# Kernel optimization log

Hardware: AMD Instinct MI355X
Metric: run time of the kernel (lower is better)

The kernel has to match this reference:

```python
import jax, jax.numpy as jnp
import numpy as np

N = 50000
E = 800000
EPS = 1e-5
# per-layer (in_dim, heads, out_dim, concat) matching GraphEncoder defaults
LAYERS = [(16, 4, 32, True), (128, 4, 32, True), (128, 4, 32, True), (128, 1, 128, False)]


def setup_inputs() -> dict:
    key = jax.random.key(0)
    ks = jax.random.split(key, 32)
    rn = lambda k, shape: jax.random.normal(k, shape, jnp.float32) * 0.1
    inp = {}
    inp["node_types"] = jax.random.randint(ks[0], (N,), 0, 3)
    inp["edge_index"] = jax.random.randint(ks[1], (2, E), 0, N)
    inp["emb"] = rn(ks[2], (3, 16))
    i = 3
    for li, (ind, h, od, _) in enumerate(LAYERS):
        inp[f"Wl{li}"] = rn(ks[i], (ind, h * od)); i += 1
        inp[f"Wr{li}"] = rn(ks[i], (ind, h * od)); i += 1
        inp[f"att{li}"] = rn(ks[i], (h, od)); i += 1
        inp[f"b{li}"] = rn(ks[i], (h * od if li < 3 else od,)); i += 1
    inp["ln_g"] = jnp.ones((4, 128), jnp.float32)
    inp["ln_b"] = jnp.zeros((4, 128), jnp.float32)
    return inp


def gatv2_layer(x, src, dst, Wl, Wr, att, b, heads, out_dim, concat):
    # PyG GATv2Conv (share_weights=False, negative_slope=0.2, self-loops added by caller)
    n = x.shape[0]
    xl = (x @ Wl).reshape(n, heads, out_dim)  # source transform (messages)
    xr = (x @ Wr).reshape(n, heads, out_dim)  # target transform
    e = jax.nn.leaky_relu(xl[src] + xr[dst], 0.2)          # [E', H, D]
    logit = jnp.einsum('ehd,hd->eh', e, att)               # [E', H]
    lmax = jax.ops.segment_max(logit, dst, num_segments=n)  # segment softmax over dst
    p = jnp.exp(logit - lmax[dst])
    z = jax.ops.segment_sum(p, dst, num_segments=n)
    alpha = p / z[dst]                                      # every node has a self-loop -> z > 0
    out = jax.ops.segment_sum(xl[src] * alpha[..., None], dst, num_segments=n)  # [n, H, D]
    out = out.reshape(n, heads * out_dim) if concat else out.mean(axis=1)
    return out + b


def layer_norm(x, g, b):
    mu = x.mean(-1, keepdims=True)
    var = ((x - mu) ** 2).mean(-1, keepdims=True)
    return (x - mu) / jnp.sqrt(var + EPS) * g + b


def reference(node_types, edge_index, emb, Wl0, Wr0, att0, b0, Wl1, Wr1, att1, b1,
              Wl2, Wr2, att2, b2, Wl3, Wr3, att3, b3, ln_g, ln_b):
    n = node_types.shape[0]
    loops = jnp.arange(n)
    src = jnp.concatenate([edge_index[0], loops])
    dst = jnp.concatenate([edge_index[1], loops])
    x = emb[node_types]
    params = [(Wl0, Wr0, att0, b0), (Wl1, Wr1, att1, b1), (Wl2, Wr2, att2, b2), (Wl3, Wr3, att3, b3)]
    for li, ((Wl, Wr, att, b), (_, h, od, concat)) in enumerate(zip(params, LAYERS)):
        res = x
        x = gatv2_layer(x, src, dst, Wl, Wr, att, b, h, od, concat)
        if x.shape[-1] == res.shape[-1]:
            x = x + res
        x = jax.nn.relu(layer_norm(x, ln_g[li], ln_b[li]))
    return x
```

## Files before the change

### kernel.cpp

```cpp
#include <hip/hip_runtime.h>

__global__ void GraphEncoder_20555713479231_kernel() {}

using hfrag8 = __attribute__((ext_vector_type(8))) _Float16;
using facc4  = __attribute__((ext_vector_type(4))) float;
using h2     = __attribute__((ext_vector_type(2))) _Float16;

__device__ __forceinline__ unsigned short f2h_bits(float f) {
  union { _Float16 h; unsigned short u; } c;
  c.h = (_Float16)f;
  return c.u;
}
__device__ __forceinline__ unsigned packh(float a, float b) {
  return (unsigned)f2h_bits(a) | ((unsigned)f2h_bits(b) << 16);
}
__device__ __forceinline__ h2 u2h(unsigned u) {
  union { unsigned u; h2 h; } c;
  c.u = u;
  return c.h;
}
__device__ __forceinline__ unsigned h22u(h2 h) {
  union { h2 h; unsigned u; } c;
  c.h = h;
  return c.u;
}
__device__ __forceinline__ float h2f_lo(unsigned u) { return (float)u2h(u).x; }
__device__ __forceinline__ float h2f_hi(unsigned u) { return (float)u2h(u).y; }

__global__ __launch_bounds__(256) void k_hist(const int* __restrict__ dst,
                                              int* __restrict__ deg, int e) {
  int i = blockIdx.x * blockDim.x + threadIdx.x;
  if (i < e) atomicAdd(&deg[dst[i]], 1);
}

__global__ __launch_bounds__(256) void k_scan1(const int* __restrict__ deg,
                                               int* __restrict__ off,
                                               int* __restrict__ bsum, int n) {
  __shared__ int wsum[4];
  int tid = threadIdx.x;
  int gid = blockIdx.x * 256 + tid;
  int lane = tid & 63, wid = tid >> 6;
  int v = (gid < n) ? (deg[gid] + 1) : 0;
  int x = v;
  #pragma unroll
  for (int d = 1; d < 64; d <<= 1) {
    int t = __shfl_up(x, d);
    if (lane >= d) x += t;
  }
  if (lane == 63) wsum[wid] = x;
  __syncthreads();
  int wpre = 0;
  for (int k = 0; k < wid; ++k) wpre += wsum[k];
  if (gid < n) off[gid] = wpre + x - v;
  if (tid == 0) {
    int t = 0;
    #pragma unroll
    for (int k = 0; k < 4; ++k) t += wsum[k];
    bsum[blockIdx.x] = t;
  }
}

__global__ __launch_bounds__(256) void k_scan2(int* __restrict__ bsum,
                                               int* __restrict__ off, int nb, int n) {
  __shared__ int wsum[4];
  int tid = threadIdx.x;
  int lane = tid & 63, wid = tid >> 6;
  int v = (tid < nb) ? bsum[tid] : 0;
  int x = v;
  #pragma unroll
  for (int d = 1; d < 64; d <<= 1) {
    int t = __shfl_up(x, d);
    if (lane >= d) x += t;
  }
  if (lane == 63) wsum[wid] = x;
  __syncthreads();
  int wpre = 0;
  for (int k = 0; k < wid; ++k) wpre += wsum[k];
  if (tid < nb) bsum[tid] = wpre + x - v;
  if (tid == 0) {
    int t = 0;
    #pragma unroll
    for (int k = 0; k < 4; ++k) t += wsum[k];
    off[n] = t;
  }
}

__global__ __launch_bounds__(256) void k_scan3(int* __restrict__ off,
                                               const int* __restrict__ bsum,
                                               int* __restrict__ pos,
                                               int* __restrict__ csr, int n) {
  int gid = blockIdx.x * 256 + threadIdx.x;
  if (gid < n) {
    int o = off[gid] + bsum[blockIdx.x];
    off[gid] = o;
    csr[o] = gid;
    pos[gid] = o + 1;
  }
}

__global__ __launch_bounds__(256) void k_fill(const int* __restrict__ src,
                                              const int* __restrict__ dst,
                                              int* __restrict__ pos,
                                              int* __restrict__ csr, int e) {
  int i = blockIdx.x * blockDim.x + threadIdx.x;
  if (i < e) {
    int d = dst[i];
    int p = atomicAdd(&pos[d], 1);
    csr[p] = src[i];
  }
}

__global__ __launch_bounds__(256)
void k_pack3(const float* __restrict__ wl1, const float* __restrict__ wr1,
             const float* __restrict__ wl2, const float* __restrict__ wr2,
             const float* __restrict__ wl3, const float* __restrict__ wr3,
             const float* __restrict__ emb,
             const float* __restrict__ wl0, const float* __restrict__ wr0,
             const int* __restrict__ types, int n,
             unsigned short* __restrict__ bp,
             unsigned* __restrict__ tlb, float* __restrict__ trf,
             unsigned* __restrict__ ptypes) {
  int b = blockIdx.x;
  if (b < 384) {
    int idx = b * 256 + threadIdx.x;
    int layer = idx >> 15;
    int r = idx & 32767;
    int j = r & 7, lane = (r >> 3) & 63, ct = (r >> 9) & 15, t = r >> 13;
    int k = t * 32 + (lane >> 4) * 8 + j;
    int c = ct * 16 + (lane & 15);
    const float* wl = (layer == 0) ? wl1 : ((layer == 1) ? wl2 : wl3);
    const float* wr = (layer == 0) ? wr1 : ((layer == 1) ? wr2 : wr3);
    float v = (c < 128) ? wl[k * 128 + c] : wr[k * 128 + (c - 128)];
    bp[idx] = f2h_bits(v);
  } else if (b == 384) {
    int tid = threadIdx.x;
    if (tid >= 192) return;
    int row = tid >> 6, cp = tid & 63, c0 = cp * 2;
    float al0 = 0.f, al1 = 0.f, ar0 = 0.f, ar1 = 0.f;
    #pragma unroll
    for (int k = 0; k < 16; ++k) {
      float ev = emb[row * 16 + k];
      al0 += ev * wl0[k * 128 + c0];
      al1 += ev * wl0[k * 128 + c0 + 1];
      ar0 += ev * wr0[k * 128 + c0];
      ar1 += ev * wr0[k * 128 + c0 + 1];
    }
    tlb[row * 64 + cp] = packh(al0, al1);
    *(float2*)(trf + row * 128 + c0) = make_float2(ar0, ar1);
  } else {
    int i = (b - 385) * 256 + threadIdx.x;
    int npk = (n + 15) >> 4;
    if (i < npk) {
      unsigned pw = 0;
      #pragma unroll
      for (int j = 0; j < 16; ++j) {
        int u = i * 16 + j;
        int ty = (u < n) ? (types[u] & 3) : 3;
        pw |= ((unsigned)ty) << (2 * j);
      }
      ptypes[i] = pw;
    }
  }
}

__global__ __launch_bounds__(256)
void k_agg0(const int* __restrict__ off, const int* __restrict__ csr,
            const unsigned* __restrict__ ptypes,
            const unsigned* __restrict__ tlb, const float* __restrict__ trf,
            const float* __restrict__ att, const float* __restrict__ bias,
            const float* __restrict__ lng, const float* __restrict__ lnb,
            unsigned* __restrict__ yout, int n) {
  int v = (blockIdx.x * blockDim.x + threadIdx.x) >> 6;
  int lane = threadIdx.x & 63;
  if (v >= n) return;
  v = __builtin_amdgcn_readfirstlane(v);
  int beg = off[v], end = off[v + 1];
  int c0 = 0, c1 = 0, c2 = 0;
  for (int base = beg; base < end; base += 64) {
    int e = base + lane;
    bool act = e < end;
    int u = act ? csr[e] : 0;
    unsigned pw = ptypes[u >> 4];
    int ty = act ? (int)((pw >> ((u & 15) * 2)) & 3) : 3;
    c0 += __popcll(__ballot(ty == 0));
    c1 += __popcll(__ballot(ty == 1));
    c2 += __popcll(__ballot(ty == 2));
  }
  float cnt[3] = {(float)c0, (float)c1, (float)c2};
  int f0 = lane * 2;
  unsigned pwv = ptypes[v >> 4];
  int tyv = (int)((pwv >> ((v & 15) * 2)) & 3);
  float2 xrv = *(const float2*)(trf + tyv * 128 + f0);
  float a0 = att[f0], a1 = att[f0 + 1];
  float s = 0.f, O0 = 0.f, O1 = 0.f;
  #pragma unroll
  for (int ty = 0; ty < 3; ++ty) {
    unsigned p = tlb[ty * 64 + lane];
    float x0 = h2f_lo(p), x1 = h2f_hi(p);
    float t0 = x0 + xrv.x; t0 = t0 > 0.f ? t0 : 0.2f * t0;
    float t1 = x1 + xrv.y; t1 = t1 > 0.f ? t1 : 0.2f * t1;
    float c = t0 * a0 + t1 * a1;
    c += __shfl_xor(c, 1);
    c += __shfl_xor(c, 2);
    c += __shfl_xor(c, 4);
    c += __shfl_xor(c, 8);
    float w = cnt[ty] * __expf(c);
    s += w;
    O0 = fmaf(w, x0, O0);
    O1 = fmaf(w, x1, O1);
  }
  float inv = 1.f / s;
  float o0 = O0 * inv + bias[f0];
  float o1 = O1 * inv + bias[f0 + 1];
  float sum = o0 + o1, sq = o0 * o0 + o1 * o1;
  #pragma unroll
  for (int d2 = 1; d2 < 64; d2 <<= 1) {
    sum += __shfl_xor(sum, d2);
    sq += __shfl_xor(sq, d2);
  }
  float mu = sum * (1.f / 128.f);
  float var = sq * (1.f / 128.f) - mu * mu;
  float rstd = rsqrtf(var + 1e-5f);
  float y0 = fmaxf((o0 - mu) * rstd * lng[f0] + lnb[f0], 0.f);
  float y1 = fmaxf((o1 - mu) * rstd * lng[f0 + 1] + lnb[f0 + 1], 0.f);
  yout[(size_t)v * 64 + lane] = packh(y0, y1);
}

__global__ __launch_bounds__(256)
void k_gemm(const unsigned* __restrict__ x, const unsigned short* __restrict__ bp,
            unsigned* __restrict__ xlo, unsigned* __restrict__ xro, int nstrips, int n) {
  int wave = (blockIdx.x * 256 + threadIdx.x) >> 6;
  int lane = threadIdx.x & 63;
  if (wave >= nstrips) return;
  int r0 = wave * 16;
  int row = r0 + (lane & 15);
  if (row >= n) row = n - 1;
  int quad = lane >> 4;
  const unsigned* ap = x + (size_t)row * 64;
  hfrag8 a[4];
  #pragma unroll
  for (int t = 0; t < 4; ++t) a[t] = *(const hfrag8*)(ap + t * 16 + quad * 4);
  unsigned short* xloS = (unsigned short*)xlo;
  unsigned short* xroS = (unsigned short*)xro;
  int rbase = r0 + quad * 4;
  #pragma unroll
  for (int ct = 0; ct < 16; ++ct) {
    facc4 acc = {0.f, 0.f, 0.f, 0.f};
    #pragma unroll
    for (int t = 0; t < 4; ++t) {
      hfrag8 b = *(const hfrag8*)(bp + (size_t)(((t * 16 + ct) * 64 + lane) * 8));
      acc = __builtin_amdgcn_mfma_f32_16x16x32_f16(a[t], b, acc, 0, 0, 0);
    }
    int col = (ct & 7) * 16 + (lane & 15);
    unsigned short* dstp = (ct < 8) ? xloS : xroS;
    #pragma unroll
    for (int i = 0; i < 4; ++i) {
      int r = rbase + i;
      if (r < n) dstp[(size_t)r * 128 + col] = f2h_bits(acc[i]);
    }
  }
}

__global__ __launch_bounds__(256)
void k_agg(const int* __restrict__ off, const int* __restrict__ csr,
           const unsigned* __restrict__ xl, const unsigned* __restrict__ xr,
           const float* __restrict__ att, const float* __restrict__ bias,
           const unsigned* __restrict__ xres,
           const float* __restrict__ lng, const float* __restrict__ lnb,
           unsigned* __restrict__ ybf, float* __restrict__ yf32, int n, int wide) {
  int v = (blockIdx.x * blockDim.x + threadIdx.x) >> 6;
  int lane = threadIdx.x & 63;
  if (v >= n) return;
  v = __builtin_amdgcn_readfirstlane(v);
  int f0 = lane * 2;
  h2 a2;
  a2.x = (_Float16)att[f0];
  a2.y = (_Float16)att[f0 + 1];
  h2 r2 = u2h(xr[(size_t)v * 64 + lane]);
  h2 k02 = {(_Float16)0.2f, (_Float16)0.2f};
  int beg = off[v], end = off[v + 1];
  int last = end - 1;
  const unsigned* xlp = xl + lane;
  int iA = csr[beg];
  int iB = csr[min(beg + 1, last)];
  int iC = csr[min(beg + 2, last)];
  int iD = csr[min(beg + 3, last)];
  unsigned pA = xlp[(size_t)iA * 64];
  unsigned pB = xlp[(size_t)iB * 64];
  unsigned pC = xlp[(size_t)iC * 64];
  unsigned pD = xlp[(size_t)iD * 64];
  float sa = 0.f, sb = 0.f;
  h2 Oa = {(_Float16)0.f, (_Float16)0.f};
  h2 Ob = {(_Float16)0.f, (_Float16)0.f};
  for (int e = beg; e < end; e += 2) {
    int i4 = csr[min(e + 4, last)];
    int i5 = csr[min(e + 5, last)];
    unsigned p4 = xlp[(size_t)i4 * 64];
    unsigned p5 = xlp[(size_t)i5 * 64];
    h2 xa = u2h(pA), xb = u2h(pB);
    h2 ta = xa + r2;
    h2 tb = xb + r2;
    h2 la = __builtin_elementwise_max(ta, ta * k02);
    h2 lb = __builtin_elementwise_max(tb, tb * k02);
    h2 da = la * a2;
    h2 db = lb * a2;
    h2 cp;
    cp.x = da.x + da.y;
    cp.y = db.x + db.y;
    unsigned cu = h22u(cp);
    cu = h22u(u2h(cu) + u2h((unsigned)__shfl_xor((int)cu, 1)));
    cu = h22u(u2h(cu) + u2h((unsigned)__shfl_xor((int)cu, 2)));
    cu = h22u(u2h(cu) + u2h((unsigned)__shfl_xor((int)cu, 4)));
    cu = h22u(u2h(cu) + u2h((unsigned)__shfl_xor((int)cu, 8)));
    if (wide) {
      cu = h22u(u2h(cu) + u2h((unsigned)__shfl_xor((int)cu, 16)));
      cu = h22u(u2h(cu) + u2h((unsigned)__shfl_xor((int)cu, 32)));
    }
    h2 cf = u2h(cu);
    float wa = __expf((float)cf.x);
    float wb = (e + 1 < end) ? __expf((float)cf.y) : 0.f;
    sa += wa;
    sb += wb;
    _Float16 wah = (_Float16)wa;
    _Float16 wbh = (_Float16)wb;
    h2 wa2 = {wah, wah};
    h2 wb2 = {wbh, wbh};
    Oa = wa2 * xa + Oa;
    Ob = wb2 * xb + Ob;
    pA = pC; pB = pD; pC = p4; pD = p5;
  }
  float s = sa + sb;
  float O0 = (float)Oa.x + (float)Ob.x;
  float O1 = (float)Oa.y + (float)Ob.y;
  float inv = 1.f / s;
  float o0 = O0 * inv + bias[f0];
  float o1 = O1 * inv + bias[f0 + 1];
  if (xres) {
    unsigned rs = xres[(size_t)v * 64 + lane];
    o0 += h2f_lo(rs);
    o1 += h2f_hi(rs);
  }
  float sum = o0 + o1, sq = o0 * o0 + o1 * o1;
  #pragma unroll
  for (int d2 = 1; d2 < 64; d2 <<= 1) {
    sum += __shfl_xor(sum, d2);
    sq += __shfl_xor(sq, d2);
  }
  float mu = sum * (1.f / 128.f);
  float var = sq * (1.f / 128.f) - mu * mu;
  float rstd = rsqrtf(var + 1e-5f);
  float y0 = fmaxf((o0 - mu) * rstd * lng[f0] + lnb[f0], 0.f);
  float y1 = fmaxf((o1 - mu) * rstd * lng[f0 + 1] + lnb[f0 + 1], 0.f);
  if (yf32) {
    *(float2*)(yf32 + (size_t)v * 128 + f0) = make_float2(y0, y1);
  } else {
    ybf[(size_t)v * 64 + lane] = packh(y0, y1);
  }
}

extern "C" void kernel_launch(void* const* d_in, const int* in_sizes, int n_in,
                              void* d_out, int out_size, void* d_ws, size_t ws_size,
                              hipStream_t stream) {
  (void)n_in; (void)out_size; (void)ws_size;
  const int* node_types = (const int*)d_in[0];
  const int* edge_index = (const int*)d_in[1];
  const float* emb = (const float*)d_in[2];
  const float* Wl0 = (const float*)d_in[3];
  const float* Wr0 = (const float*)d_in[4];
  const float* att0 = (const float*)d_in[5];
  const float* b0 = (const float*)d_in[6];
  const float* Wl1 = (const float*)d_in[7];
  const float* Wr1 = (const float*)d_in[8];
  const float* att1 = (const float*)d_in[9];
  const float* b1 = (const float*)d_in[10];
  const float* Wl2 = (const float*)d_in[11];
  const float* Wr2 = (const float*)d_in[12];
  const float* att2 = (const float*)d_in[13];
  const float* b2 = (const float*)d_in[14];
  const float* Wl3 = (const float*)d_in[15];
  const float* Wr3 = (const float*)d_in[16];
  const float* att3 = (const float*)d_in[17];
  const float* b3 = (const float*)d_in[18];
  const float* lng = (const float*)d_in[19];
  const float* lnb = (const float*)d_in[20];

  int n = in_sizes[0];
  int e = in_sizes[1] / 2;
  const int* srcp = edge_index;
  const int* dstp = edge_index + e;
  int nblocks = (n + 255) / 256;

  char* wsp = (char*)d_ws;
  size_t ofs = 0;
  int* deg = (int*)(wsp + ofs); ofs += (((size_t)n * 4) + 255) & ~(size_t)255;
  int* off = (int*)(wsp + ofs); ofs += (((size_t)(n + 1) * 4) + 255) & ~(size_t)255;
  int* csr = (int*)(wsp + ofs); ofs += (((size_t)(e + n) * 4) + 255) & ~(size_t)255;
  int* bsum = (int*)(wsp + ofs); ofs += (((size_t)nblocks * 4) + 255) & ~(size_t)255;
  unsigned* xlb = (unsigned*)(wsp + ofs); ofs += (((size_t)n * 64 * 4) + 255) & ~(size_t)255;
  unsigned* xrb = (unsigned*)(wsp + ofs); ofs += (((size_t)n * 64 * 4) + 255) & ~(size_t)255;
  unsigned* xcur = (unsigned*)(wsp + ofs); ofs += (((size_t)n * 64 * 4) + 255) & ~(size_t)255;
  unsigned short* bp = (unsigned short*)(wsp + ofs); ofs += 3 * 65536;
  unsigned* tlb = (unsigned*)(wsp + ofs); ofs += 1024;
  float* trf = (float*)(wsp + ofs); ofs += 2048;
  unsigned* ptypes = (unsigned*)(wsp + ofs); ofs += ((((size_t)(n + 15) / 16) * 4) + 255) & ~(size_t)255;
  int* pos = deg;

  (void)hipMemsetAsync(deg, 0, (size_t)n * 4, stream);
  k_hist<<<(e + 255) / 256, 256, 0, stream>>>(dstp, deg, e);
  int npk = (n + 15) / 16;
  int packGrid = 385 + (npk + 255) / 256;
  k_pack3<<<packGrid, 256, 0, stream>>>(Wl1, Wr1, Wl2, Wr2, Wl3, Wr3,
                                        emb, Wl0, Wr0, node_types, n,
                                        bp, tlb, trf, ptypes);
  k_scan1<<<nblocks, 256, 0, stream>>>(deg, off, bsum, n);
  k_scan2<<<1, 256, 0, stream>>>(bsum, off, nblocks, n);
  k_scan3<<<nblocks, 256, 0, stream>>>(off, bsum, pos, csr, n);
  k_fill<<<(e + 255) / 256, 256, 0, stream>>>(srcp, dstp, pos, csr, e);

  int aggBlocks = (n * 64 + 255) / 256;

  k_agg0<<<aggBlocks, 256, 0, stream>>>(off, csr, ptypes, tlb, trf,
                                        att0, b0, lng, lnb, xcur, n);

  int nstrips = (n + 15) / 16;
  int gemmBlocks = (nstrips + 3) / 4;

  k_gemm<<<gemmBlocks, 256, 0, stream>>>(xcur, bp, xlb, xrb, nstrips, n);
  k_agg<<<aggBlocks, 256, 0, stream>>>(off, csr, xlb, xrb, att1, b1, xcur,
                                       lng + 128, lnb + 128, xcur, (float*)0, n, 0);
  k_gemm<<<gemmBlocks, 256, 0, stream>>>(xcur, bp + 32768, xlb, xrb, nstrips, n);
  k_agg<<<aggBlocks, 256, 0, stream>>>(off, csr, xlb, xrb, att2, b2, xcur,
                                       lng + 256, lnb + 256, xcur, (float*)0, n, 0);
  k_gemm<<<gemmBlocks, 256, 0, stream>>>(xcur, bp + 65536, xlb, xrb, nstrips, n);
  k_agg<<<aggBlocks, 256, 0, stream>>>(off, csr, xlb, xrb, att3, b3, xcur,
                                       lng + 384, lnb + 384, (unsigned*)0, (float*)d_out, n, 1);
}
```

Baseline: 418.5 us.

## Batch neighbor indices per wave and deepen gather prefetch in aggregation

The aggregation kernel now loads up to 64 CSR neighbor indices with one coalesced wave load and broadcasts each with readlane, so it no longer issues a scalar index load per edge. It processes four edges per iteration, interleaves two shuffle reductions, and keeps eight row gathers in flight instead of four. The wide/narrow head reduction becomes a template parameter, so the runtime branch goes away. The cost is higher register pressure and extra clamped redundant loads at the tail of each chunk for low-degree nodes (average degree is about 17).

```diff
diff --git a/kernel.cpp b/kernel.cpp
--- a/kernel.cpp
+++ b/kernel.cpp
@@ -26,6 +26,13 @@
 }
 __device__ __forceinline__ float h2f_lo(unsigned u) { return (float)u2h(u).x; }
 __device__ __forceinline__ float h2f_hi(unsigned u) { return (float)u2h(u).y; }
+
+__device__ __forceinline__ int rl(int v, int l) {
+  return __builtin_amdgcn_readlane(v, l);
+}
+__device__ __forceinline__ unsigned grow(const unsigned* __restrict__ p, int idx, int lane) {
+  return p[(((unsigned)idx) << 6) + (unsigned)lane];
+}
 
 __global__ __launch_bounds__(256) void k_hist(const int* __restrict__ dst,
                                               int* __restrict__ deg, int e) {
@@ -261,13 +268,14 @@
   }
 }
 
+template <int WIDE>
 __global__ __launch_bounds__(256)
-void k_agg(const int* __restrict__ off, const int* __restrict__ csr,
-           const unsigned* __restrict__ xl, const unsigned* __restrict__ xr,
-           const float* __restrict__ att, const float* __restrict__ bias,
-           const unsigned* __restrict__ xres,
-           const float* __restrict__ lng, const float* __restrict__ lnb,
-           unsigned* __restrict__ ybf, float* __restrict__ yf32, int n, int wide) {
+void k_agg_t(const int* __restrict__ off, const int* __restrict__ csr,
+             const unsigned* __restrict__ xl, const unsigned* __restrict__ xr,
+             const float* __restrict__ att, const float* __restrict__ bias,
+             const unsigned* __restrict__ xres,
+             const float* __restrict__ lng, const float* __restrict__ lnb,
+             unsigned* __restrict__ ybf, float* __restrict__ yf32, int n) {
   int v = (blockIdx.x * blockDim.x + threadIdx.x) >> 6;
   int lane = threadIdx.x & 63;
   if (v >= n) return;
@@ -279,62 +287,83 @@
   h2 r2 = u2h(xr[(size_t)v * 64 + lane]);
   h2 k02 = {(_Float16)0.2f, (_Float16)0.2f};
   int beg = off[v], end = off[v + 1];
-  int last = end - 1;
-  const unsigned* xlp = xl + lane;
-  int iA = csr[beg];
-  int iB = csr[min(beg + 1, last)];
-  int iC = csr[min(beg + 2, last)];
-  int iD = csr[min(beg + 3, last)];
-  unsigned pA = xlp[(size_t)iA * 64];
-  unsigned pB = xlp[(size_t)iB * 64];
-  unsigned pC = xlp[(size_t)iC * 64];
-  unsigned pD = xlp[(size_t)iD * 64];
-  float sa = 0.f, sb = 0.f;
-  h2 Oa = {(_Float16)0.f, (_Float16)0.f};
-  h2 Ob = {(_Float16)0.f, (_Float16)0.f};
-  for (int e = beg; e < end; e += 2) {
-    int i4 = csr[min(e + 4, last)];
-    int i5 = csr[min(e + 5, last)];
-    unsigned p4 = xlp[(size_t)i4 * 64];
-    unsigned p5 = xlp[(size_t)i5 * 64];
-    h2 xa = u2h(pA), xb = u2h(pB);
-    h2 ta = xa + r2;
-    h2 tb = xb + r2;
-    h2 la = __builtin_elementwise_max(ta, ta * k02);
-    h2 lb = __builtin_elementwise_max(tb, tb * k02);
-    h2 da = la * a2;
-    h2 db = lb * a2;
-    h2 cp;
-    cp.x = da.x + da.y;
-    cp.y = db.x + db.y;
-    unsigned cu = h22u(cp);
-    cu = h22u(u2h(cu) + u2h((unsigned)__shfl_xor((int)cu, 1)));
-    cu = h22u(u2h(cu) + u2h((unsigned)__shfl_xor((int)cu, 2)));
-    cu = h22u(u2h(cu) + u2h((unsigned)__shfl_xor((int)cu, 4)));
-    cu = h22u(u2h(cu) + u2h((unsigned)__shfl_xor((int)cu, 8)));
-    if (wide) {
-      cu = h22u(u2h(cu) + u2h((unsigned)__shfl_xor((int)cu, 16)));
-      cu = h22u(u2h(cu) + u2h((unsigned)__shfl_xor((int)cu, 32)));
+  float s0 = 0.f, s1 = 0.f;
+  h2 O0 = {(_Float16)0.f, (_Float16)0.f};
+  h2 O1 = O0, O2 = O0, O3 = O0;
+
+  for (int base = beg; base < end; base += 64) {
+    int m = end - base;
+    if (m > 64) m = 64;
+    int last = m - 1;
+    int idxv = csr[base + (lane < m ? lane : last)];
+    int ng = (m + 3) >> 2;
+    unsigned c0 = grow(xl, rl(idxv, 0), lane);
+    unsigned c1 = grow(xl, rl(idxv, min(1, last)), lane);
+    unsigned c2 = grow(xl, rl(idxv, min(2, last)), lane);
+    unsigned c3 = grow(xl, rl(idxv, min(3, last)), lane);
+    unsigned n0 = grow(xl, rl(idxv, min(4, last)), lane);
+    unsigned n1 = grow(xl, rl(idxv, min(5, last)), lane);
+    unsigned n2 = grow(xl, rl(idxv, min(6, last)), lane);
+    unsigned n3 = grow(xl, rl(idxv, min(7, last)), lane);
+    for (int g = 0; g < ng; ++g) {
+      int jb = g * 4;
+      int pb = jb + 8;
+      unsigned t0 = grow(xl, rl(idxv, min(pb + 0, last)), lane);
+      unsigned t1 = grow(xl, rl(idxv, min(pb + 1, last)), lane);
+      unsigned t2 = grow(xl, rl(idxv, min(pb + 2, last)), lane);
+      unsigned t3 = grow(xl, rl(idxv, min(pb + 3, last)), lane);
+      h2 xa = u2h(c0), xb = u2h(c1), xc = u2h(c2), xd = u2h(c3);
+      h2 ta = xa + r2, tb = xb + r2, tc = xc + r2, td = xd + r2;
+      h2 la = __builtin_elementwise_max(ta, ta * k02);
+      h2 lb = __builtin_elementwise_max(tb, tb * k02);
+      h2 lc = __builtin_elementwise_max(tc, tc * k02);
+      h2 ld = __builtin_elementwise_max(td, td * k02);
+      h2 da = la * a2, db = lb * a2, dc = lc * a2, dd = ld * a2;
+      h2 cp0, cp1;
+      cp0.x = da.x + da.y;
+      cp0.y = db.x + db.y;
+      cp1.x = dc.x + dc.y;
+      cp1.y = dd.x + dd.y;
+      unsigned cu0 = h22u(cp0), cu1 = h22u(cp1);
+      cu0 = h22u(u2h(cu0) + u2h((unsigned)__shfl_xor((int)cu0, 1)));
+      cu1 = h22u(u2h(cu1) + u2h((unsigned)__shfl_xor((int)cu1, 1)));
+      cu0 = h22u(u2h(cu0) + u2h((unsigned)__shfl_xor((int)cu0, 2)));
+      cu1 = h22u(u2h(cu1) + u2h((unsigned)__shfl_xor((int)cu1, 2)));
+      cu0 = h22u(u2h(cu0) + u2h((unsigned)__shfl_xor((int)cu0, 4)));
+      cu1 = h22u(u2h(cu1) + u2h((unsigned)__shfl_xor((int)cu1, 4)));
+      cu0 = h22u(u2h(cu0) + u2h((unsigned)__shfl_xor((int)cu0, 8)));
+      cu1 = h22u(u2h(cu1) + u2h((unsigned)__shfl_xor((int)cu1, 8)));
+      if (WIDE) {
+        cu0 = h22u(u2h(cu0) + u2h((unsigned)__shfl_xor((int)cu0, 16)));
+        cu1 = h22u(u2h(cu1) + u2h((unsigned)__shfl_xor((int)cu1, 16)));
+        cu0 = h22u(u2h(cu0) + u2h((unsigned)__shfl_xor((int)cu0, 32)));
+        cu1 = h22u(u2h(cu1) + u2h((unsigned)__shfl_xor((int)cu1, 32)));
+      }
+      h2 cf0 = u2h(cu0), cf1 = u2h(cu1);
+      float wa = (jb + 0 < m) ? __expf((float)cf0.x) : 0.f;
+      float wb = (jb + 1 < m) ? __expf((float)cf0.y) : 0.f;
+      float wc = (jb + 2 < m) ? __expf((float)cf1.x) : 0.f;
+      float wd = (jb + 3 < m) ? __expf((float)cf1.y) : 0.f;
+      s0 += wa + wb;
+      s1 += wc + wd;
+      _Float16 wah = (_Float16)wa, wbh = (_Float16)wb;
+      _Float16 wch = (_Float16)wc, wdh = (_Float16)wd;
+      h2 wa2 = {wah, wah}, wb2 = {wbh, wbh};
+      h2 wc2 = {wch, wch}, wd2 = {wdh, wdh};
+      O0 = wa2 * xa + O0;
+      O1 = wb2 * xb + O1;
+      O2 = wc2 * xc + O2;
+      O3 = wd2 * xd + O3;
+      c0 = n0; c1 = n1; c2 = n2; c3 = n3;
+      n0 = t0; n1 = t1; n2 = t2; n3 = t3;
     }
-    h2 cf = u2h(cu);
-    float wa = __expf((float)cf.x);
-    float wb = (e + 1 < end) ? __expf((float)cf.y) : 0.f;
-    sa += wa;
-    sb += wb;
-    _Float16 wah = (_Float16)wa;
-    _Float16 wbh = (_Float16)wb;
-    h2 wa2 = {wah, wah};
-    h2 wb2 = {wbh, wbh};
-    Oa = wa2 * xa + Oa;
-    Ob = wb2 * xb + Ob;
-    pA = pC; pB = pD; pC = p4; pD = p5;
-  }
-  float s = sa + sb;
-  float O0 = (float)Oa.x + (float)Ob.x;
-  float O1 = (float)Oa.y + (float)Ob.y;
+  }
+  float s = s0 + s1;
+  float Ox = (float)O0.x + (float)O1.x + (float)O2.x + (float)O3.x;
+  float Oy = (float)O0.y + (float)O1.y + (float)O2.y + (float)O3.y;
   float inv = 1.f / s;
-  float o0 = O0 * inv + bias[f0];
-  float o1 = O1 * inv + bias[f0 + 1];
+  float o0 = Ox * inv + bias[f0];
+  float o1 = Oy * inv + bias[f0 + 1];
   if (xres) {
     unsigned rs = xres[(size_t)v * 64 + lane];
     o0 += h2f_lo(rs);
@@ -426,12 +455,12 @@
   int gemmBlocks = (nstrips + 3) / 4;
 
   k_gemm<<<gemmBlocks, 256, 0, stream>>>(xcur, bp, xlb, xrb, nstrips, n);
-  k_agg<<<aggBlocks, 256, 0, stream>>>(off, csr, xlb, xrb, att1, b1, xcur,
-                                       lng + 128, lnb + 128, xcur, (float*)0, n, 0);
+  k_agg_t<0><<<aggBlocks, 256, 0, stream>>>(off, csr, xlb, xrb, att1, b1, xcur,
+                                            lng + 128, lnb + 128, xcur, (float*)0, n);
   k_gemm<<<gemmBlocks, 256, 0, stream>>>(xcur, bp + 32768, xlb, xrb, nstrips, n);
-  k_agg<<<aggBlocks, 256, 0, stream>>>(off, csr, xlb, xrb, att2, b2, xcur,
-                                       lng + 256, lnb + 256, xcur, (float*)0, n, 0);
+  k_agg_t<0><<<aggBlocks, 256, 0, stream>>>(off, csr, xlb, xrb, att2, b2, xcur,
+                                            lng + 256, lnb + 256, xcur, (float*)0, n);
   k_gemm<<<gemmBlocks, 256, 0, stream>>>(xcur, bp + 65536, xlb, xrb, nstrips, n);
-  k_agg<<<aggBlocks, 256, 0, stream>>>(off, csr, xlb, xrb, att3, b3, xcur,
-                                       lng + 384, lnb + 384, (unsigned*)0, (float*)d_out, n, 1);
-}
+  k_agg_t<1><<<aggBlocks, 256, 0, stream>>>(off, csr, xlb, xrb, att3, b3, xcur,
+                                            lng + 384, lnb + 384, (unsigned*)0, (float*)d_out, n);
+}
```

Result: no change. 417.6 us (-0.2%).

## Precompute layer-0 type-pair weights, count source types in histogram, merge scans

Applied to the files above, without the earlier changes.

Layer 0 inputs depend only on node type, so the attention weight for each (target type, source type) pair is precomputed once into a small table. Per-node source-type counts are accumulated with packed atomics in the histogram pass, which removes the per-edge CSR walk in the layer-0 aggregation. The second and third scan kernels are merged into one that recomputes block prefixes redundantly, the memset is folded into the pack kernel, and exp is replaced by exp2 with log2e folded into the attention vector. The cost is extra atomics and a types gather in the histogram pass, plus 16-bit packed counters that can overflow if one node has 65536 or more neighbours of a single type.

```diff
diff --git a/kernel.cpp b/kernel.cpp
--- a/kernel.cpp
+++ b/kernel.cpp
@@ -27,10 +27,19 @@
 __device__ __forceinline__ float h2f_lo(unsigned u) { return (float)u2h(u).x; }
 __device__ __forceinline__ float h2f_hi(unsigned u) { return (float)u2h(u).y; }
 
-__global__ __launch_bounds__(256) void k_hist(const int* __restrict__ dst,
-                                              int* __restrict__ deg, int e) {
+#define LOG2E 1.4426950408889634f
+
+__global__ __launch_bounds__(256) void k_hist(const int* __restrict__ src,
+                                              const int* __restrict__ dst,
+                                              const int* __restrict__ types,
+                                              int* __restrict__ deg,
+                                              unsigned* __restrict__ h01, int e) {
   int i = blockIdx.x * blockDim.x + threadIdx.x;
-  if (i < e) atomicAdd(&deg[dst[i]], 1);
+  if (i >= e) return;
+  int d = dst[i];
+  atomicAdd(&deg[d], 1);
+  int ty = types[src[i]] & 3;
+  if (ty < 2) atomicAdd(&h01[d], ty == 0 ? 1u : 65536u);
 }
 
 __global__ __launch_bounds__(256) void k_scan1(const int* __restrict__ deg,
@@ -60,41 +69,37 @@
   }
 }
 
-__global__ __launch_bounds__(256) void k_scan2(int* __restrict__ bsum,
-                                               int* __restrict__ off, int nb, int n) {
-  __shared__ int wsum[4];
-  int tid = threadIdx.x;
-  int lane = tid & 63, wid = tid >> 6;
-  int v = (tid < nb) ? bsum[tid] : 0;
-  int x = v;
+__global__ __launch_bounds__(256) void k_scan23(int* __restrict__ off,
+                                                const int* __restrict__ bsum,
+                                                int* __restrict__ pos,
+                                                int* __restrict__ csr, int nb, int n) {
+  __shared__ int sh[8];
+  int tid = threadIdx.x, lane = tid & 63, wid = tid >> 6;
+  int p = 0, t = 0;
+  for (int k = tid; k < nb; k += 256) {
+    int bv = bsum[k];
+    t += bv;
+    if (k < (int)blockIdx.x) p += bv;
+  }
   #pragma unroll
   for (int d = 1; d < 64; d <<= 1) {
-    int t = __shfl_up(x, d);
-    if (lane >= d) x += t;
-  }
-  if (lane == 63) wsum[wid] = x;
+    p += __shfl_xor(p, d);
+    t += __shfl_xor(t, d);
+  }
+  if (lane == 0) { sh[wid] = p; sh[4 + wid] = t; }
   __syncthreads();
-  int wpre = 0;
-  for (int k = 0; k < wid; ++k) wpre += wsum[k];
-  if (tid < nb) bsum[tid] = wpre + x - v;
-  if (tid == 0) {
-    int t = 0;
-    #pragma unroll
-    for (int k = 0; k < 4; ++k) t += wsum[k];
-    off[n] = t;
-  }
-}
-
-__global__ __launch_bounds__(256) void k_scan3(int* __restrict__ off,
-                                               const int* __restrict__ bsum,
-                                               int* __restrict__ pos,
-                                               int* __restrict__ csr, int n) {
-  int gid = blockIdx.x * 256 + threadIdx.x;
+  p = sh[0] + sh[1] + sh[2] + sh[3];
+  t = sh[4] + sh[5] + sh[6] + sh[7];
+  int gid = blockIdx.x * 256 + tid;
   if (gid < n) {
-    int o = off[gid] + bsum[blockIdx.x];
+    int o = off[gid] + p;
     off[gid] = o;
     csr[o] = gid;
     pos[gid] = o + 1;
+  }
+  if (blockIdx.x == 0) {
+    if (tid == 0) off[n] = t;
+    if (tid < 16) csr[t + tid] = 0;
   }
 }
 
@@ -116,10 +121,10 @@
              const float* __restrict__ wl3, const float* __restrict__ wr3,
              const float* __restrict__ emb,
              const float* __restrict__ wl0, const float* __restrict__ wr0,
-             const int* __restrict__ types, int n,
+             const float* __restrict__ att0, int n,
              unsigned short* __restrict__ bp,
-             unsigned* __restrict__ tlb, float* __restrict__ trf,
-             unsigned* __restrict__ ptypes) {
+             unsigned* __restrict__ tlb, float* __restrict__ w0tab,
+             int* __restrict__ deg, unsigned* __restrict__ h01) {
   int b = blockIdx.x;
   if (b < 384) {
     int idx = b * 256 + threadIdx.x;
@@ -133,81 +138,79 @@
     float v = (c < 128) ? wl[k * 128 + c] : wr[k * 128 + (c - 128)];
     bp[idx] = f2h_bits(v);
   } else if (b == 384) {
+    __shared__ float stl[384], str[384];
     int tid = threadIdx.x;
-    if (tid >= 192) return;
-    int row = tid >> 6, cp = tid & 63, c0 = cp * 2;
-    float al0 = 0.f, al1 = 0.f, ar0 = 0.f, ar1 = 0.f;
-    #pragma unroll
-    for (int k = 0; k < 16; ++k) {
-      float ev = emb[row * 16 + k];
-      al0 += ev * wl0[k * 128 + c0];
-      al1 += ev * wl0[k * 128 + c0 + 1];
-      ar0 += ev * wr0[k * 128 + c0];
-      ar1 += ev * wr0[k * 128 + c0 + 1];
+    if (tid < 192) {
+      int row = tid >> 6, cp = tid & 63, c0 = cp * 2;
+      float al0 = 0.f, al1 = 0.f, ar0 = 0.f, ar1 = 0.f;
+      #pragma unroll
+      for (int k = 0; k < 16; ++k) {
+        float ev = emb[row * 16 + k];
+        al0 += ev * wl0[k * 128 + c0];
+        al1 += ev * wl0[k * 128 + c0 + 1];
+        ar0 += ev * wr0[k * 128 + c0];
+        ar1 += ev * wr0[k * 128 + c0 + 1];
+      }
+      tlb[row * 64 + cp] = packh(al0, al1);
+      stl[row * 128 + c0] = al0; stl[row * 128 + c0 + 1] = al1;
+      str[row * 128 + c0] = ar0; str[row * 128 + c0 + 1] = ar1;
     }
-    tlb[row * 64 + cp] = packh(al0, al1);
-    *(float2*)(trf + row * 128 + c0) = make_float2(ar0, ar1);
+    __syncthreads();
+    if (tid < 192) {
+      int tyv = tid >> 6, lane = tid & 63, f0 = lane * 2;
+      float xr0 = str[tyv * 128 + f0], xr1 = str[tyv * 128 + f0 + 1];
+      float a0 = att0[f0] * LOG2E, a1 = att0[f0 + 1] * LOG2E;
+      #pragma unroll
+      for (int ty = 0; ty < 3; ++ty) {
+        float x0 = stl[ty * 128 + f0], x1 = stl[ty * 128 + f0 + 1];
+        float t0 = x0 + xr0; t0 = t0 > 0.f ? t0 : 0.2f * t0;
+        float t1 = x1 + xr1; t1 = t1 > 0.f ? t1 : 0.2f * t1;
+        float c = t0 * a0 + t1 * a1;
+        c += __shfl_xor(c, 1);
+        c += __shfl_xor(c, 2);
+        c += __shfl_xor(c, 4);
+        c += __shfl_xor(c, 8);
+        if ((lane & 15) == 0)
+          w0tab[(tyv * 3 + ty) * 4 + (lane >> 4)] = __builtin_amdgcn_exp2f(c);
+      }
+    }
   } else {
     int i = (b - 385) * 256 + threadIdx.x;
-    int npk = (n + 15) >> 4;
-    if (i < npk) {
-      unsigned pw = 0;
-      #pragma unroll
-      for (int j = 0; j < 16; ++j) {
-        int u = i * 16 + j;
-        int ty = (u < n) ? (types[u] & 3) : 3;
-        pw |= ((unsigned)ty) << (2 * j);
-      }
-      ptypes[i] = pw;
-    }
+    if (i < n) { deg[i] = 0; h01[i] = 0u; }
   }
 }
 
 __global__ __launch_bounds__(256)
-void k_agg0(const int* __restrict__ off, const int* __restrict__ csr,
-            const unsigned* __restrict__ ptypes,
-            const unsigned* __restrict__ tlb, const float* __restrict__ trf,
-            const float* __restrict__ att, const float* __restrict__ bias,
-            const float* __restrict__ lng, const float* __restrict__ lnb,
-            unsigned* __restrict__ yout, int n) {
+void k_agg0h(const int* __restrict__ off, const unsigned* __restrict__ h01,
+             const int* __restrict__ types,
+             const unsigned* __restrict__ tlb, const float* __restrict__ w0tab,
+             const float* __restrict__ bias,
+             const float* __restrict__ lng, const float* __restrict__ lnb,
+             unsigned* __restrict__ yout, int n) {
   int v = (blockIdx.x * blockDim.x + threadIdx.x) >> 6;
   int lane = threadIdx.x & 63;
   if (v >= n) return;
   v = __builtin_amdgcn_readfirstlane(v);
   int beg = off[v], end = off[v + 1];
-  int c0 = 0, c1 = 0, c2 = 0;
-  for (int base = beg; base < end; base += 64) {
-    int e = base + lane;
-    bool act = e < end;
-    int u = act ? csr[e] : 0;
-    unsigned pw = ptypes[u >> 4];
-    int ty = act ? (int)((pw >> ((u & 15) * 2)) & 3) : 3;
-    c0 += __popcll(__ballot(ty == 0));
-    c1 += __popcll(__ballot(ty == 1));
-    c2 += __popcll(__ballot(ty == 2));
-  }
-  float cnt[3] = {(float)c0, (float)c1, (float)c2};
+  int m = end - beg;
+  unsigned hc = h01[v];
+  int tyv = types[v] & 3;
+  float cnt[3];
+  int c0 = (int)(hc & 0xffffu), c1 = (int)(hc >> 16);
+  cnt[0] = (float)c0;
+  cnt[1] = (float)c1;
+  cnt[2] = (float)((m - 1) - c0 - c1);
+  cnt[tyv] += 1.f;
+  int head = lane >> 4;
   int f0 = lane * 2;
-  unsigned pwv = ptypes[v >> 4];
-  int tyv = (int)((pwv >> ((v & 15) * 2)) & 3);
-  float2 xrv = *(const float2*)(trf + tyv * 128 + f0);
-  float a0 = att[f0], a1 = att[f0 + 1];
   float s = 0.f, O0 = 0.f, O1 = 0.f;
   #pragma unroll
   for (int ty = 0; ty < 3; ++ty) {
+    float w = cnt[ty] * w0tab[(tyv * 3 + ty) * 4 + head];
     unsigned p = tlb[ty * 64 + lane];
-    float x0 = h2f_lo(p), x1 = h2f_hi(p);
-    float t0 = x0 + xrv.x; t0 = t0 > 0.f ? t0 : 0.2f * t0;
-    float t1 = x1 + xrv.y; t1 = t1 > 0.f ? t1 : 0.2f * t1;
-    float c = t0 * a0 + t1 * a1;
-    c += __shfl_xor(c, 1);
-    c += __shfl_xor(c, 2);
-    c += __shfl_xor(c, 4);
-    c += __shfl_xor(c, 8);
-    float w = cnt[ty] * __expf(c);
     s += w;
-    O0 = fmaf(w, x0, O0);
-    O1 = fmaf(w, x1, O1);
+    O0 = fmaf(w, h2f_lo(p), O0);
+    O1 = fmaf(w, h2f_hi(p), O1);
   }
   float inv = 1.f / s;
   float o0 = O0 * inv + bias[f0];
@@ -274,8 +277,8 @@
   v = __builtin_amdgcn_readfirstlane(v);
   int f0 = lane * 2;
   h2 a2;
-  a2.x = (_Float16)att[f0];
-  a2.y = (_Float16)att[f0 + 1];
+  a2.x = (_Float16)(att[f0] * LOG2E);
+  a2.y = (_Float16)(att[f0 + 1] * LOG2E);
   h2 r2 = u2h(xr[(size_t)v * 64 + lane]);
   h2 k02 = {(_Float16)0.2f, (_Float16)0.2f};
   int beg = off[v], end = off[v + 1];
@@ -317,8 +320,8 @@
       cu = h22u(u2h(cu) + u2h((unsigned)__shfl_xor((int)cu, 32)));
     }
     h2 cf = u2h(cu);
-    float wa = __expf((float)cf.x);
-    float wb = (e + 1 < end) ? __expf((float)cf.y) : 0.f;
+    float wa = __builtin_amdgcn_exp2f((float)cf.x);
+    float wb = (e + 1 < end) ? __builtin_amdgcn_exp2f((float)cf.y) : 0.f;
     sa += wa;
     sb += wb;
     _Float16 wah = (_Float16)wa;
@@ -394,33 +397,30 @@
   size_t ofs = 0;
   int* deg = (int*)(wsp + ofs); ofs += (((size_t)n * 4) + 255) & ~(size_t)255;
   int* off = (int*)(wsp + ofs); ofs += (((size_t)(n + 1) * 4) + 255) & ~(size_t)255;
-  int* csr = (int*)(wsp + ofs); ofs += (((size_t)(e + n) * 4) + 255) & ~(size_t)255;
+  int* csr = (int*)(wsp + ofs); ofs += (((size_t)(e + n + 64) * 4) + 255) & ~(size_t)255;
   int* bsum = (int*)(wsp + ofs); ofs += (((size_t)nblocks * 4) + 255) & ~(size_t)255;
+  unsigned* h01 = (unsigned*)(wsp + ofs); ofs += (((size_t)n * 4) + 255) & ~(size_t)255;
   unsigned* xlb = (unsigned*)(wsp + ofs); ofs += (((size_t)n * 64 * 4) + 255) & ~(size_t)255;
   unsigned* xrb = (unsigned*)(wsp + ofs); ofs += (((size_t)n * 64 * 4) + 255) & ~(size_t)255;
   unsigned* xcur = (unsigned*)(wsp + ofs); ofs += (((size_t)n * 64 * 4) + 255) & ~(size_t)255;
   unsigned short* bp = (unsigned short*)(wsp + ofs); ofs += 3 * 65536;
   unsigned* tlb = (unsigned*)(wsp + ofs); ofs += 1024;
-  float* trf = (float*)(wsp + ofs); ofs += 2048;
-  unsigned* ptypes = (unsigned*)(wsp + ofs); ofs += ((((size_t)(n + 15) / 16) * 4) + 255) & ~(size_t)255;
+  float* w0tab = (float*)(wsp + ofs); ofs += 256;
   int* pos = deg;
 
-  (void)hipMemsetAsync(deg, 0, (size_t)n * 4, stream);
-  k_hist<<<(e + 255) / 256, 256, 0, stream>>>(dstp, deg, e);
-  int npk = (n + 15) / 16;
-  int packGrid = 385 + (npk + 255) / 256;
+  int packGrid = 385 + nblocks;
   k_pack3<<<packGrid, 256, 0, stream>>>(Wl1, Wr1, Wl2, Wr2, Wl3, Wr3,
-                                        emb, Wl0, Wr0, node_types, n,
-                                        bp, tlb, trf, ptypes);
+                                        emb, Wl0, Wr0, att0, n,
+                                        bp, tlb, w0tab, deg, h01);
+  k_hist<<<(e + 255) / 256, 256, 0, stream>>>(srcp, dstp, node_types, deg, h01, e);
   k_scan1<<<nblocks, 256, 0, stream>>>(deg, off, bsum, n);
-  k_scan2<<<1, 256, 0, stream>>>(bsum, off, nblocks, n);
-  k_scan3<<<nblocks, 256, 0, stream>>>(off, bsum, pos, csr, n);
+  k_scan23<<<nblocks, 256, 0, stream>>>(off, bsum, pos, csr, nblocks, n);
   k_fill<<<(e + 255) / 256, 256, 0, stream>>>(srcp, dstp, pos, csr, e);
 
   int aggBlocks = (n * 64 + 255) / 256;
 
-  k_agg0<<<aggBlocks, 256, 0, stream>>>(off, csr, ptypes, tlb, trf,
-                                        att0, b0, lng, lnb, xcur, n);
+  k_agg0h<<<aggBlocks, 256, 0, stream>>>(off, h01, node_types, tlb, w0tab,
+                                         b0, lng, lnb, xcur, n);
 
   int nstrips = (n + 15) / 16;
   int gemmBlocks = (nstrips + 3) / 4;
```

Result: no change. 421.1 us (+0.6%).
